# Optimization experiments

Hardware: AMD Instinct MI355X
Metric: run time of the kernel (lower is better)

## Reference

```python
import jax, jax.numpy as jnp
import numpy as np

B, T, C, HD = 4, 2048, 1024, 64

def setup_inputs() -> dict:
    key = jax.random.key(0)
    kx, kq, kk, kv = jax.random.split(key, 4)
    # Weights stored as [n_embed, head_size]; equivalent to torch Linear weight transposed.
    scale = 1.0 / np.sqrt(C)
    return {
        "x": jax.random.normal(kx, (B, T, C), dtype=jnp.float32),
        "Wq": jax.random.normal(kq, (C, HD), dtype=jnp.float32) * scale,
        "Wk": jax.random.normal(kk, (C, HD), dtype=jnp.float32) * scale,
        "Wv": jax.random.normal(kv, (C, HD), dtype=jnp.float32) * scale,
    }

def reference(x, Wq, Wk, Wv):
    # Projections (no bias)
    q = x @ Wq  # [B,T,HD]
    k = x @ Wk
    v = x @ Wv
    hd = k.shape[-1]
    # NOTE: original multiplies by sqrt(head_size) (not the usual 1/sqrt) -- faithful.
    scores = jnp.einsum("btd,bsd->bts", q, k) * (hd ** 0.5)  # [B,T,T]
    # First softmax over full (unmasked) rows
    w = jax.nn.softmax(scores, axis=-1)
    # Causal mask applied AFTER the first softmax, then a second softmax
    causal = jnp.tril(jnp.ones((q.shape[1], q.shape[1]), dtype=bool))  # [T,T]
    w = jnp.where(causal[None, :, :], w, -jnp.inf)
    w = jax.nn.softmax(w, axis=-1)
    out = jnp.einsum("bts,bsd->btd", w, v)  # [B,T,HD]
    return out
```

## Files before the change

### kernel.cpp

```cpp
#include <hip/hip_runtime.h>
#include <math.h>

#define T_  2048
#define C_  1024
#define HD_ 64

typedef __attribute__((ext_vector_type(8))) short bf16x8;
typedef __attribute__((ext_vector_type(4))) float f32x4;

#define MFMA_BF16(A, B, C) __builtin_amdgcn_mfma_f32_16x16x32_bf16(A, B, C, 0, 0, 0)

__device__ __forceinline__ short f2bf(float f) {
    union { float f; unsigned u; } v; v.f = f;
    unsigned r = v.u + 0x7fffu + ((v.u >> 16) & 1u);
    return (short)(r >> 16);
}
__device__ __forceinline__ float bf2f(short s) {
    union { float f; unsigned u; } v;
    v.u = ((unsigned)(unsigned short)s) << 16;
    return v.f;
}

__global__ __launch_bounds__(256) void prep_w_kernel(
    const float* __restrict__ Wq, const float* __restrict__ Wk,
    const float* __restrict__ Wv, short* __restrict__ wt)
{
    const int m = blockIdx.y;
    const float* W = (m == 0) ? Wq : (m == 1) ? Wk : Wv;
    const int t = threadIdx.x;
    const int c = blockIdx.x * 64 + (t >> 2);
    const int hg = (t & 3) * 16;
    const float4* wp = (const float4*)(W + (size_t)c * HD_ + hg);
    short* hi = wt + (size_t)(m * 2 + 0) * 64 * 1024;
    short* lo = wt + (size_t)(m * 2 + 1) * 64 * 1024;
    #pragma unroll
    for (int u = 0; u < 4; ++u) {
        float4 f = wp[u];
        float vs[4] = {f.x, f.y, f.z, f.w};
        #pragma unroll
        for (int e = 0; e < 4; ++e) {
            int h = hg + u * 4 + e;
            short hh = f2bf(vs[e]);
            hi[(size_t)h * 1024 + c] = hh;
            lo[(size_t)h * 1024 + c] = f2bf(vs[e] - bf2f(hh));
        }
    }
}

__global__ __launch_bounds__(256) void qkv_proj_kernel(
    const float* __restrict__ x, const short* __restrict__ wt,
    short* __restrict__ qhp, short* __restrict__ qlp,
    short* __restrict__ khp, short* __restrict__ klp,
    short* __restrict__ vtp)
{
    __shared__ __align__(16) short xh[32 * 64], xl[32 * 64];
    __shared__ __align__(16) short wh[192 * 64], wl[192 * 64];

    const int t = threadIdx.x, L = t & 63, wv = t >> 6;
    const int R0 = blockIdx.x * 32;
    const int xrow = t >> 3, xch = t & 7;

    f32x4 acc[2][3];
    #pragma unroll
    for (int i = 0; i < 2; ++i)
        #pragma unroll
        for (int j = 0; j < 3; ++j) acc[i][j] = {0.f, 0.f, 0.f, 0.f};

    float4 xa0, xa1;
    bf16x8 wr[2][6];
    const float* xp = x + (size_t)(R0 + xrow) * C_ + xch * 8;

    auto loadX = [&](int c0) {
        xa0 = *(const float4*)(xp + c0);
        xa1 = *(const float4*)(xp + c0 + 4);
    };
    auto loadW = [&](int c0) {
        #pragma unroll
        for (int pl = 0; pl < 2; ++pl)
            #pragma unroll
            for (int u = 0; u < 6; ++u) {
                int cc = t + 256 * u;
                int row = cc >> 3, ch = cc & 7;
                int m = row >> 6, h = row & 63;
                wr[pl][u] = *(const bf16x8*)(wt + (size_t)(m * 2 + pl) * 65536
                                             + (size_t)h * 1024 + c0 + ch * 8);
            }
    };

    loadX(0); loadW(0);
    for (int c0 = 0; c0 < C_; c0 += 64) {
        __syncthreads();
        {
            float vs[8] = {xa0.x, xa0.y, xa0.z, xa0.w, xa1.x, xa1.y, xa1.z, xa1.w};
            bf16x8 vh, vl;
            #pragma unroll
            for (int e = 0; e < 8; ++e) {
                short hh = f2bf(vs[e]);
                vh[e] = hh;
                vl[e] = f2bf(vs[e] - bf2f(hh));
            }
            int slot = (xch ^ (xrow & 7)) * 8;
            *(bf16x8*)&xh[xrow * 64 + slot] = vh;
            *(bf16x8*)&xl[xrow * 64 + slot] = vl;
        }
        {
            #pragma unroll
            for (int pl = 0; pl < 2; ++pl)
                #pragma unroll
                for (int u = 0; u < 6; ++u) {
                    int cc = t + 256 * u;
                    int row = cc >> 3, ch = cc & 7;
                    short* dst = pl ? wl : wh;
                    *(bf16x8*)&dst[row * 64 + ((ch ^ (row & 7)) * 8)] = wr[pl][u];
                }
        }
        if (c0 + 64 < C_) { loadX(c0 + 64); loadW(c0 + 64); }
        __syncthreads();
        #pragma unroll
        for (int kc = 0; kc < 2; ++kc) {
            const int ch = kc * 4 + (L >> 4);
            bf16x8 axh[2], axl[2], bwh[3], bwl[3];
            #pragma unroll
            for (int rt = 0; rt < 2; ++rt) {
                int row = rt * 16 + (L & 15);
                int off = row * 64 + ((ch ^ (row & 7)) * 8);
                axh[rt] = *(const bf16x8*)&xh[off];
                axl[rt] = *(const bf16x8*)&xl[off];
            }
            #pragma unroll
            for (int cl = 0; cl < 3; ++cl) {
                int ct = wv + cl * 4;
                int wrow = ct * 16 + (L & 15);
                int off = wrow * 64 + ((ch ^ (wrow & 7)) * 8);
                bwh[cl] = *(const bf16x8*)&wh[off];
                bwl[cl] = *(const bf16x8*)&wl[off];
            }
            #pragma unroll
            for (int rt = 0; rt < 2; ++rt) {
                acc[rt][0] = MFMA_BF16(axl[rt], bwh[0], acc[rt][0]);
                acc[rt][0] = MFMA_BF16(axh[rt], bwl[0], acc[rt][0]);
                acc[rt][0] = MFMA_BF16(axh[rt], bwh[0], acc[rt][0]);
                acc[rt][1] = MFMA_BF16(axl[rt], bwh[1], acc[rt][1]);
                acc[rt][1] = MFMA_BF16(axh[rt], bwl[1], acc[rt][1]);
                acc[rt][1] = MFMA_BF16(axh[rt], bwh[1], acc[rt][1]);
                acc[rt][2] = MFMA_BF16(bwh[2], axh[rt], acc[rt][2]);
            }
        }
    }

    const int quad = L >> 4;
    #pragma unroll
    for (int rt = 0; rt < 2; ++rt) {
        #pragma unroll
        for (int r = 0; r < 4; ++r) {
            int row = R0 + rt * 16 + quad * 4 + r;
            int h = wv * 16 + (L & 15);
            float vq = acc[rt][0][r] * 8.f;
            short hq = f2bf(vq);
            qhp[(size_t)row * HD_ + h] = hq;
            qlp[(size_t)row * HD_ + h] = f2bf(vq - bf2f(hq));
            float vk = acc[rt][1][r];
            short hk = f2bf(vk);
            khp[(size_t)row * HD_ + h] = hk;
            klp[(size_t)row * HD_ + h] = f2bf(vk - bf2f(hk));
            int d = wv * 16 + quad * 4 + r;
            int tt = R0 + rt * 16 + (L & 15);
            int bb = tt >> 11, tl = tt & (T_ - 1);
            vtp[(size_t)(bb * 64 + d) * T_ + tl] = f2bf(acc[rt][2][r]);
        }
    }
}

__global__ __launch_bounds__(256) void stats_kernel(
    const short* __restrict__ qhp, const short* __restrict__ qlp,
    const short* __restrict__ khp, const short* __restrict__ klp,
    float* __restrict__ pm)
{
    __shared__ __align__(16) short khs[64 * 64], kls[64 * 64];
    __shared__ float red[4 * 64 * 2];

    const int t = threadIdx.x, L = t & 63, wv = t >> 6;
    const int bt = blockIdx.x, seg = blockIdx.y, b = blockIdx.z;
    const int R0 = bt * 64, S0 = seg * 512;

    bf16x8 qfh[4][2], qfl[4][2];
    #pragma unroll
    for (int rt = 0; rt < 4; ++rt)
        #pragma unroll
        for (int dc = 0; dc < 2; ++dc) {
            int row = R0 + rt * 16 + (L & 15);
            size_t off = ((size_t)b * T_ + row) * HD_ + dc * 32 + (L >> 4) * 8;
            qfh[rt][dc] = *(const bf16x8*)(qhp + off);
            qfl[rt][dc] = *(const bf16x8*)(qlp + off);
        }

    float ml[4][4], ll[4][4];
    #pragma unroll
    for (int rt = 0; rt < 4; ++rt)
        #pragma unroll
        for (int r = 0; r < 4; ++r) { ml[rt][r] = -1e30f; ll[rt][r] = 0.f; }

    const int pl = t >> 7, id = t & 127;
    for (int jt = 0; jt < 8; ++jt) {
        __syncthreads();
        {
            const short* src = pl ? klp : khp;
            short* dst = pl ? kls : khs;
            #pragma unroll
            for (int u = 0; u < 4; ++u) {
                int cid = id * 4 + u;
                int col = cid >> 3, ch = cid & 7;
                bf16x8 v = *(const bf16x8*)(src
                    + ((size_t)b * T_ + S0 + jt * 64 + col) * HD_ + ch * 8);
                *(bf16x8*)&dst[col * 64 + ((ch ^ (col & 7)) * 8)] = v;
            }
        }
        __syncthreads();
        const int colL = wv * 16 + (L & 15);
        bf16x8 kf[2], kfl[2];
        #pragma unroll
        for (int dc = 0; dc < 2; ++dc) {
            int ch = dc * 4 + (L >> 4);
            int off = colL * 64 + ((ch ^ (colL & 7)) * 8);
            kf[dc]  = *(const bf16x8*)&khs[off];
            kfl[dc] = *(const bf16x8*)&kls[off];
        }
        #pragma unroll
        for (int rt = 0; rt < 4; ++rt) {
            f32x4 s = {0.f, 0.f, 0.f, 0.f};
            #pragma unroll
            for (int dc = 0; dc < 2; ++dc) {
                s = MFMA_BF16(qfl[rt][dc], kf[dc], s);
                s = MFMA_BF16(qfh[rt][dc], kfl[dc], s);
                s = MFMA_BF16(qfh[rt][dc], kf[dc], s);
            }
            #pragma unroll
            for (int r = 0; r < 4; ++r) {
                float mn = fmaxf(ml[rt][r], s[r]);
                ll[rt][r] = ll[rt][r] * __expf(ml[rt][r] - mn) + __expf(s[r] - mn);
                ml[rt][r] = mn;
            }
        }
    }
    #pragma unroll
    for (int off = 1; off < 16; off <<= 1)
        #pragma unroll
        for (int rt = 0; rt < 4; ++rt)
            #pragma unroll
            for (int r = 0; r < 4; ++r) {
                float mo = __shfl_xor(ml[rt][r], off, 64);
                float lo = __shfl_xor(ll[rt][r], off, 64);
                float mn = fmaxf(ml[rt][r], mo);
                ll[rt][r] = ll[rt][r] * __expf(ml[rt][r] - mn) + lo * __expf(mo - mn);
                ml[rt][r] = mn;
            }
    if ((L & 15) == 0) {
        #pragma unroll
        for (int rt = 0; rt < 4; ++rt)
            #pragma unroll
            for (int r = 0; r < 4; ++r) {
                int row = rt * 16 + (L >> 4) * 4 + r;
                red[(wv * 64 + row) * 2 + 0] = ml[rt][r];
                red[(wv * 64 + row) * 2 + 1] = ll[rt][r];
            }
    }
    __syncthreads();
    if (t < 64) {
        float M = red[t * 2], S = red[t * 2 + 1];
        #pragma unroll
        for (int w = 1; w < 4; ++w) {
            float mo = red[(w * 64 + t) * 2], lo = red[(w * 64 + t) * 2 + 1];
            float mn = fmaxf(M, mo);
            S = S * __expf(M - mn) + lo * __expf(mo - mn);
            M = mn;
        }
        size_t o = ((size_t)((b * 32 + bt) * 4 + seg) * 64 + t) * 2;
        pm[o] = M;
        pm[o + 1] = S;
    }
}

__global__ __launch_bounds__(256) void stat_merge_kernel(
    const float* __restrict__ pm, float* __restrict__ msp, float* __restrict__ ilp)
{
    int gid = blockIdx.x * 256 + threadIdx.x;
    int b = gid >> 11, rl = gid & 2047, bt = rl >> 6, rr = rl & 63;
    float M = -1e30f, S = 0.f;
    #pragma unroll
    for (int seg = 0; seg < 4; ++seg) {
        size_t o = ((size_t)((b * 32 + bt) * 4 + seg) * 64 + rr) * 2;
        float mo = pm[o], lo = pm[o + 1];
        float mn = fmaxf(M, mo);
        S = S * __expf(M - mn) + lo * __expf(mo - mn);
        M = mn;
    }
    msp[gid] = M;
    ilp[gid] = 1.f / S;
}

__global__ __launch_bounds__(512) void pv_kernel(
    const short* __restrict__ qhp, const short* __restrict__ qlp,
    const short* __restrict__ khp, const short* __restrict__ klp,
    const short* __restrict__ vtp, const float* __restrict__ msp,
    const float* __restrict__ ilp, float* __restrict__ out)
{
    __shared__ __align__(16) short khs[128 * 64];
    __shared__ __align__(16) short kls[128 * 64];
    __shared__ __align__(16) short vts[64 * 128];
    __shared__ __align__(16) float es[32 * 128];

    const int t = threadIdx.x, L = t & 63, wv = t >> 6;
    const int b = blockIdx.x >> 6, p = blockIdx.x & 63;
    const int IA = p * 16, IB = (127 - p) * 16;

    bf16x8 qfh[2][2], qfl[2][2];
    #pragma unroll
    for (int rt = 0; rt < 2; ++rt) {
        int row = (rt ? IB : IA) + (L & 15);
        const short* qb  = qhp + ((size_t)b * T_ + row) * HD_;
        const short* qbl = qlp + ((size_t)b * T_ + row) * HD_;
        #pragma unroll
        for (int dc = 0; dc < 2; ++dc) {
            int off = dc * 32 + (L >> 4) * 8;
            qfh[rt][dc] = *(const bf16x8*)(qb + off);
            qfl[rt][dc] = *(const bf16x8*)(qbl + off);
        }
    }
    float ms[2][4], is[2][4];
    int rowg[2][4];
    #pragma unroll
    for (int rt = 0; rt < 2; ++rt)
        #pragma unroll
        for (int r = 0; r < 4; ++r) {
            int rg = (rt ? IB : IA) + (L >> 4) * 4 + r;
            rowg[rt][r] = rg;
            ms[rt][r] = msp[b * T_ + rg];
            is[rt][r] = ilp[b * T_ + rg];
        }

    const short* kbh = khp + (size_t)b * T_ * HD_;
    const short* kbl = klp + (size_t)b * T_ * HD_;
    const short* vb  = vtp + (size_t)b * 64 * T_;
    const int spl = t >> 8, sid = t & 255;

    auto stageK = [&](int jt) {
        const short* src = spl ? kbl : kbh;
        short* dst = spl ? kls : khs;
        #pragma unroll
        for (int u = 0; u < 4; ++u) {
            int cid = sid * 4 + u;
            int col = cid >> 3, c8 = cid & 7;
            bf16x8 v = *(const bf16x8*)(src + (size_t)(jt * 128 + col) * HD_ + c8 * 8);
            *(bf16x8*)&dst[col * 64 + ((c8 ^ (col & 7)) * 8)] = v;
        }
    };
    auto stageV = [&](int jt) {
        #pragma unroll
        for (int u = 0; u < 2; ++u) {
            int cid = t + u * 512;
            int d = cid >> 4, ch = cid & 15;
            bf16x8 v = *(const bf16x8*)(vb + (size_t)d * T_ + jt * 128 + ch * 8);
            *(bf16x8*)&vts[d * 128 + ((ch ^ ((d & 7) * 2)) * 8)] = v;
        }
    };

    const int nA = (IA + 143) >> 7;
    const int nB = (IB + 143) >> 7;
    const int rtp = wv & 1, dh = (wv >> 1) & 1, khf = wv >> 2;
    f32x4 ov[2];
    ov[0] = {0.f, 0.f, 0.f, 0.f};
    ov[1] = {0.f, 0.f, 0.f, 0.f};
    float dn[2][4];
    #pragma unroll
    for (int rt = 0; rt < 2; ++rt)
        #pragma unroll
        for (int r = 0; r < 4; ++r) dn[rt][r] = 0.f;

    for (int jt = 0; jt < nB; ++jt) {
        __syncthreads();
        stageK(jt);
        stageV(jt);
        __syncthreads();
        const int col = wv * 16 + (L & 15);
        bf16x8 kf[2], kfl[2];
        #pragma unroll
        for (int dc = 0; dc < 2; ++dc) {
            int ch = dc * 4 + (L >> 4);
            int off = col * 64 + ((ch ^ (col & 7)) * 8);
            kf[dc]  = *(const bf16x8*)&khs[off];
            kfl[dc] = *(const bf16x8*)&kls[off];
        }
        for (int rt = 0; rt < 2; ++rt) {
            if (rt == 0 && jt >= nA) continue;
            f32x4 s = {0.f, 0.f, 0.f, 0.f};
            #pragma unroll
            for (int dc = 0; dc < 2; ++dc) {
                s = MFMA_BF16(qfl[rt][dc], kf[dc], s);
                s = MFMA_BF16(qfh[rt][dc], kfl[dc], s);
                s = MFMA_BF16(qfh[rt][dc], kf[dc], s);
            }
            #pragma unroll
            for (int r = 0; r < 4; ++r) {
                float pv = __expf(s[r] - ms[rt][r]) * is[rt][r];
                int colg = jt * 128 + col;
                float ev = (colg <= rowg[rt][r]) ? __expf(pv) : 0.f;
                dn[rt][r] += ev;
                int rid = rt * 16 + (L >> 4) * 4 + r;
                es[rid * 128 + (((col >> 3) ^ (rid & 15)) * 8) + (col & 7)] = ev;
            }
        }
        __syncthreads();
        if (!(rtp == 0 && jt >= nA)) {
            #pragma unroll
            for (int u = 0; u < 2; ++u) {
                int kc = khf * 2 + u;
                int rid = rtp * 16 + (L & 15);
                int chunk = (kc * 4 + (L >> 4)) ^ (rid & 15);
                const float* ep = &es[rid * 128 + chunk * 8];
                float4 e0 = *(const float4*)ep;
                float4 e1 = *(const float4*)(ep + 4);
                bf16x8 ef;
                ef[0] = f2bf(e0.x); ef[1] = f2bf(e0.y);
                ef[2] = f2bf(e0.z); ef[3] = f2bf(e0.w);
                ef[4] = f2bf(e1.x); ef[5] = f2bf(e1.y);
                ef[6] = f2bf(e1.z); ef[7] = f2bf(e1.w);
                #pragma unroll
                for (int dt = 0; dt < 2; ++dt) {
                    int d = dh * 32 + dt * 16 + (L & 15);
                    int ch = kc * 4 + (L >> 4);
                    bf16x8 vf = *(const bf16x8*)&vts[d * 128 + ((ch ^ ((d & 7) * 2)) * 8)];
                    ov[dt] = MFMA_BF16(ef, vf, ov[dt]);
                }
            }
        }
    }

    #pragma unroll
    for (int off = 1; off < 16; off <<= 1)
        #pragma unroll
        for (int rt = 0; rt < 2; ++rt)
            #pragma unroll
            for (int r = 0; r < 4; ++r)
                dn[rt][r] += __shfl_xor(dn[rt][r], off, 64);
    __syncthreads();
    float* red  = es + 2304;
    float* dinv = es + 2560;
    if ((L & 15) == 0) {
        #pragma unroll
        for (int rt = 0; rt < 2; ++rt)
            #pragma unroll
            for (int r = 0; r < 4; ++r) {
                int rid = rt * 16 + (L >> 4) * 4 + r;
                red[wv * 32 + rid] = dn[rt][r];
            }
    }
    __syncthreads();
    if (t < 32) {
        float D = 0.f;
        #pragma unroll
        for (int w = 0; w < 8; ++w) D += red[w * 32 + t];
        dinv[t] = 1.f / D;
    }
    float* obuf = es;
    __syncthreads();
    if (khf == 1) {
        #pragma unroll
        for (int dt = 0; dt < 2; ++dt)
            #pragma unroll
            for (int r = 0; r < 4; ++r)
                obuf[((wv - 4) * 64 + L) * 8 + dt * 4 + r] = ov[dt][r];
    }
    __syncthreads();
    if (khf == 0) {
        float* ob = out + (size_t)b * T_ * HD_;
        #pragma unroll
        for (int dt = 0; dt < 2; ++dt)
            #pragma unroll
            for (int r = 0; r < 4; ++r) {
                float o = ov[dt][r] + obuf[(wv * 64 + L) * 8 + dt * 4 + r];
                int rid = rtp * 16 + (L >> 4) * 4 + r;
                int row = (rtp ? IB : IA) + (L >> 4) * 4 + r;
                int d = dh * 32 + dt * 16 + (L & 15);
                ob[(size_t)row * HD_ + d] = o * dinv[rid];
            }
    }
}

extern "C" void kernel_launch(void* const* d_in, const int* in_sizes, int n_in,
                              void* d_out, int out_size, void* d_ws, size_t ws_size,
                              hipStream_t stream) {
    (void)in_sizes; (void)n_in; (void)out_size; (void)ws_size;
    const float* x  = (const float*)d_in[0];
    const float* Wq = (const float*)d_in[1];
    const float* Wk = (const float*)d_in[2];
    const float* Wv = (const float*)d_in[3];
    float* outp = (float*)d_out;

    char* ws = (char*)d_ws;
    short* wt  = (short*)ws;
    float* pm  = (float*)ws;
    float* msp = (float*)(ws + 262144);
    float* ilp = (float*)(ws + 294912);
    short* qh = (short*)(ws + 786432);
    short* ql = (short*)(ws + 786432 + 1048576);
    short* kh = (short*)(ws + 786432 + 2 * 1048576);
    short* kl = (short*)(ws + 786432 + 3 * 1048576);
    short* vt = (short*)(ws + 786432 + 4 * 1048576);

    prep_w_kernel<<<dim3(16, 3), 256, 0, stream>>>(Wq, Wk, Wv, wt);
    qkv_proj_kernel<<<dim3(256), 256, 0, stream>>>(x, wt, qh, ql, kh, kl, vt);
    stats_kernel<<<dim3(32, 4, 4), 256, 0, stream>>>(qh, ql, kh, kl, pm);
    stat_merge_kernel<<<dim3(32), 256, 0, stream>>>(pm, msp, ilp);
    pv_kernel<<<dim3(256), 512, 0, stream>>>(qh, ql, kh, kl, vt, msp, ilp, outp);
}
```

Before: 154.9 us.

## Materialize causal scores in stats pass and drop QK recompute from PV kernel

The stats kernel now writes the fp32 scores of the lower-triangular part to a workspace buffer while computing row statistics. It uses twice as many key segments and register-prefetches the next K tile. The PV kernel no longer recomputes the three-pass split-bf16 QK^T. Instead it reads those stored scores, applies both softmaxes and multiplies with V directly from global memory using 16-row blocks. This removes redundant MFMA work but adds roughly 32MB of score writes and reads through HBM and a larger workspace.

```diff
diff --git a/kernel.cpp b/kernel.cpp
--- a/kernel.cpp
+++ b/kernel.cpp
@@ -174,14 +174,14 @@
 __global__ __launch_bounds__(256) void stats_kernel(
     const short* __restrict__ qhp, const short* __restrict__ qlp,
     const short* __restrict__ khp, const short* __restrict__ klp,
-    float* __restrict__ pm)
+    float* __restrict__ pm, float* __restrict__ sc)
 {
     __shared__ __align__(16) short khs[64 * 64], kls[64 * 64];
     __shared__ float red[4 * 64 * 2];
 
     const int t = threadIdx.x, L = t & 63, wv = t >> 6;
     const int bt = blockIdx.x, seg = blockIdx.y, b = blockIdx.z;
-    const int R0 = bt * 64, S0 = seg * 512;
+    const int R0 = bt * 64, S0 = seg * 256;
 
     bf16x8 qfh[4][2], qfl[4][2];
     #pragma unroll
@@ -201,21 +201,30 @@
         for (int r = 0; r < 4; ++r) { ml[rt][r] = -1e30f; ll[rt][r] = 0.f; }
 
     const int pl = t >> 7, id = t & 127;
-    for (int jt = 0; jt < 8; ++jt) {
+    const short* ksrc = pl ? klp : khp;
+    short* kdst = pl ? kls : khs;
+    bf16x8 kr[4];
+    auto loadK = [&](int jt) {
+        #pragma unroll
+        for (int u = 0; u < 4; ++u) {
+            int cid = id * 4 + u;
+            int col = cid >> 3, ch = cid & 7;
+            kr[u] = *(const bf16x8*)(ksrc
+                + ((size_t)b * T_ + S0 + jt * 64 + col) * HD_ + ch * 8);
+        }
+    };
+
+    loadK(0);
+    for (int jt = 0; jt < 4; ++jt) {
         __syncthreads();
-        {
-            const short* src = pl ? klp : khp;
-            short* dst = pl ? kls : khs;
-            #pragma unroll
-            for (int u = 0; u < 4; ++u) {
-                int cid = id * 4 + u;
-                int col = cid >> 3, ch = cid & 7;
-                bf16x8 v = *(const bf16x8*)(src
-                    + ((size_t)b * T_ + S0 + jt * 64 + col) * HD_ + ch * 8);
-                *(bf16x8*)&dst[col * 64 + ((ch ^ (col & 7)) * 8)] = v;
-            }
+        #pragma unroll
+        for (int u = 0; u < 4; ++u) {
+            int cid = id * 4 + u;
+            int col = cid >> 3, ch = cid & 7;
+            *(bf16x8*)&kdst[col * 64 + ((ch ^ (col & 7)) * 8)] = kr[u];
         }
         __syncthreads();
+        if (jt < 3) loadK(jt + 1);
         const int colL = wv * 16 + (L & 15);
         bf16x8 kf[2], kfl[2];
         #pragma unroll
@@ -225,6 +234,7 @@
             kf[dc]  = *(const bf16x8*)&khs[off];
             kfl[dc] = *(const bf16x8*)&kls[off];
         }
+        const bool doStore = (S0 + jt * 64) <= (R0 + 63);
         #pragma unroll
         for (int rt = 0; rt < 4; ++rt) {
             f32x4 s = {0.f, 0.f, 0.f, 0.f};
@@ -233,6 +243,13 @@
                 s = MFMA_BF16(qfl[rt][dc], kf[dc], s);
                 s = MFMA_BF16(qfh[rt][dc], kfl[dc], s);
                 s = MFMA_BF16(qfh[rt][dc], kf[dc], s);
+            }
+            if (doStore) {
+                #pragma unroll
+                for (int r = 0; r < 4; ++r) {
+                    int row = R0 + rt * 16 + (L >> 4) * 4 + r;
+                    sc[((size_t)b * T_ + row) * T_ + S0 + jt * 64 + colL] = s[r];
+                }
             }
             #pragma unroll
             for (int r = 0; r < 4; ++r) {
@@ -274,7 +291,7 @@
             S = S * __expf(M - mn) + lo * __expf(mo - mn);
             M = mn;
         }
-        size_t o = ((size_t)((b * 32 + bt) * 4 + seg) * 64 + t) * 2;
+        size_t o = ((size_t)((b * 32 + bt) * 8 + seg) * 64 + t) * 2;
         pm[o] = M;
         pm[o + 1] = S;
     }
@@ -287,8 +304,8 @@
     int b = gid >> 11, rl = gid & 2047, bt = rl >> 6, rr = rl & 63;
     float M = -1e30f, S = 0.f;
     #pragma unroll
-    for (int seg = 0; seg < 4; ++seg) {
-        size_t o = ((size_t)((b * 32 + bt) * 4 + seg) * 64 + rr) * 2;
+    for (int seg = 0; seg < 8; ++seg) {
+        size_t o = ((size_t)((b * 32 + bt) * 8 + seg) * 64 + rr) * 2;
         float mo = pm[o], lo = pm[o + 1];
         float mn = fmaxf(M, mo);
         S = S * __expf(M - mn) + lo * __expf(mo - mn);
@@ -298,192 +315,75 @@
     ilp[gid] = 1.f / S;
 }
 
-__global__ __launch_bounds__(512) void pv_kernel(
-    const short* __restrict__ qhp, const short* __restrict__ qlp,
-    const short* __restrict__ khp, const short* __restrict__ klp,
-    const short* __restrict__ vtp, const float* __restrict__ msp,
-    const float* __restrict__ ilp, float* __restrict__ out)
+__global__ __launch_bounds__(256) void pv_kernel(
+    const float* __restrict__ sc, const short* __restrict__ vtp,
+    const float* __restrict__ msp, const float* __restrict__ ilp,
+    float* __restrict__ out)
 {
-    __shared__ __align__(16) short khs[128 * 64];
-    __shared__ __align__(16) short kls[128 * 64];
-    __shared__ __align__(16) short vts[64 * 128];
-    __shared__ __align__(16) float es[32 * 128];
+    __shared__ float ored[4][16][64];
+    __shared__ float dred[4][16];
 
     const int t = threadIdx.x, L = t & 63, wv = t >> 6;
-    const int b = blockIdx.x >> 6, p = blockIdx.x & 63;
-    const int IA = p * 16, IB = (127 - p) * 16;
-
-    bf16x8 qfh[2][2], qfl[2][2];
-    #pragma unroll
-    for (int rt = 0; rt < 2; ++rt) {
-        int row = (rt ? IB : IA) + (L & 15);
-        const short* qb  = qhp + ((size_t)b * T_ + row) * HD_;
-        const short* qbl = qlp + ((size_t)b * T_ + row) * HD_;
-        #pragma unroll
-        for (int dc = 0; dc < 2; ++dc) {
-            int off = dc * 32 + (L >> 4) * 8;
-            qfh[rt][dc] = *(const bf16x8*)(qb + off);
-            qfl[rt][dc] = *(const bf16x8*)(qbl + off);
-        }
-    }
-    float ms[2][4], is[2][4];
-    int rowg[2][4];
-    #pragma unroll
-    for (int rt = 0; rt < 2; ++rt)
-        #pragma unroll
-        for (int r = 0; r < 4; ++r) {
-            int rg = (rt ? IB : IA) + (L >> 4) * 4 + r;
-            rowg[rt][r] = rg;
-            ms[rt][r] = msp[b * T_ + rg];
-            is[rt][r] = ilp[b * T_ + rg];
-        }
-
-    const short* kbh = khp + (size_t)b * T_ * HD_;
-    const short* kbl = klp + (size_t)b * T_ * HD_;
-    const short* vb  = vtp + (size_t)b * 64 * T_;
-    const int spl = t >> 8, sid = t & 255;
-
-    auto stageK = [&](int jt) {
-        const short* src = spl ? kbl : kbh;
-        short* dst = spl ? kls : khs;
-        #pragma unroll
-        for (int u = 0; u < 4; ++u) {
-            int cid = sid * 4 + u;
-            int col = cid >> 3, c8 = cid & 7;
-            bf16x8 v = *(const bf16x8*)(src + (size_t)(jt * 128 + col) * HD_ + c8 * 8);
-            *(bf16x8*)&dst[col * 64 + ((c8 ^ (col & 7)) * 8)] = v;
-        }
-    };
-    auto stageV = [&](int jt) {
-        #pragma unroll
-        for (int u = 0; u < 2; ++u) {
-            int cid = t + u * 512;
-            int d = cid >> 4, ch = cid & 15;
-            bf16x8 v = *(const bf16x8*)(vb + (size_t)d * T_ + jt * 128 + ch * 8);
-            *(bf16x8*)&vts[d * 128 + ((ch ^ ((d & 7) * 2)) * 8)] = v;
-        }
-    };
-
-    const int nA = (IA + 143) >> 7;
-    const int nB = (IB + 143) >> 7;
-    const int rtp = wv & 1, dh = (wv >> 1) & 1, khf = wv >> 2;
-    f32x4 ov[2];
-    ov[0] = {0.f, 0.f, 0.f, 0.f};
-    ov[1] = {0.f, 0.f, 0.f, 0.f};
-    float dn[2][4];
-    #pragma unroll
-    for (int rt = 0; rt < 2; ++rt)
-        #pragma unroll
-        for (int r = 0; r < 4; ++r) dn[rt][r] = 0.f;
-
-    for (int jt = 0; jt < nB; ++jt) {
-        __syncthreads();
-        stageK(jt);
-        stageV(jt);
-        __syncthreads();
-        const int col = wv * 16 + (L & 15);
-        bf16x8 kf[2], kfl[2];
-        #pragma unroll
-        for (int dc = 0; dc < 2; ++dc) {
-            int ch = dc * 4 + (L >> 4);
-            int off = col * 64 + ((ch ^ (col & 7)) * 8);
-            kf[dc]  = *(const bf16x8*)&khs[off];
-            kfl[dc] = *(const bf16x8*)&kls[off];
-        }
-        for (int rt = 0; rt < 2; ++rt) {
-            if (rt == 0 && jt >= nA) continue;
-            f32x4 s = {0.f, 0.f, 0.f, 0.f};
-            #pragma unroll
-            for (int dc = 0; dc < 2; ++dc) {
-                s = MFMA_BF16(qfl[rt][dc], kf[dc], s);
-                s = MFMA_BF16(qfh[rt][dc], kfl[dc], s);
-                s = MFMA_BF16(qfh[rt][dc], kf[dc], s);
-            }
-            #pragma unroll
-            for (int r = 0; r < 4; ++r) {
-                float pv = __expf(s[r] - ms[rt][r]) * is[rt][r];
-                int colg = jt * 128 + col;
-                float ev = (colg <= rowg[rt][r]) ? __expf(pv) : 0.f;
-                dn[rt][r] += ev;
-                int rid = rt * 16 + (L >> 4) * 4 + r;
-                es[rid * 128 + (((col >> 3) ^ (rid & 15)) * 8) + (col & 7)] = ev;
-            }
-        }
-        __syncthreads();
-        if (!(rtp == 0 && jt >= nA)) {
-            #pragma unroll
-            for (int u = 0; u < 2; ++u) {
-                int kc = khf * 2 + u;
-                int rid = rtp * 16 + (L & 15);
-                int chunk = (kc * 4 + (L >> 4)) ^ (rid & 15);
-                const float* ep = &es[rid * 128 + chunk * 8];
-                float4 e0 = *(const float4*)ep;
-                float4 e1 = *(const float4*)(ep + 4);
-                bf16x8 ef;
-                ef[0] = f2bf(e0.x); ef[1] = f2bf(e0.y);
-                ef[2] = f2bf(e0.z); ef[3] = f2bf(e0.w);
-                ef[4] = f2bf(e1.x); ef[5] = f2bf(e1.y);
-                ef[6] = f2bf(e1.z); ef[7] = f2bf(e1.w);
-                #pragma unroll
-                for (int dt = 0; dt < 2; ++dt) {
-                    int d = dh * 32 + dt * 16 + (L & 15);
-                    int ch = kc * 4 + (L >> 4);
-                    bf16x8 vf = *(const bf16x8*)&vts[d * 128 + ((ch ^ ((d & 7) * 2)) * 8)];
-                    ov[dt] = MFMA_BF16(ef, vf, ov[dt]);
-                }
-            }
-        }
-    }
-
-    #pragma unroll
-    for (int off = 1; off < 16; off <<= 1)
-        #pragma unroll
-        for (int rt = 0; rt < 2; ++rt)
-            #pragma unroll
-            for (int r = 0; r < 4; ++r)
-                dn[rt][r] += __shfl_xor(dn[rt][r], off, 64);
+    const int b = blockIdx.x & 3;
+    const int p = 127 - (blockIdx.x >> 2);
+    const int T0 = p * 16;
+    const int row = T0 + (L & 15);
+
+    const float ms = msp[b * T_ + row];
+    const float is = ilp[b * T_ + row];
+    const float* srow = sc + ((size_t)b * T_ + row) * T_;
+    const short* vb = vtp + (size_t)b * 64 * T_;
+    const int nJ = (T0 + 143) >> 7;
+    const int cq = (L >> 4) * 8;
+
+    f32x4 ov[4];
+    #pragma unroll
+    for (int dt = 0; dt < 4; ++dt) ov[dt] = {0.f, 0.f, 0.f, 0.f};
+    float dn = 0.f;
+
+    for (int jt = 0; jt < nJ; ++jt) {
+        const int c0 = jt * 128 + wv * 32 + cq;
+        float4 s0 = *(const float4*)(srow + c0);
+        float4 s1 = *(const float4*)(srow + c0 + 4);
+        float vs[8] = {s0.x, s0.y, s0.z, s0.w, s1.x, s1.y, s1.z, s1.w};
+        bf16x8 ef;
+        #pragma unroll
+        for (int e = 0; e < 8; ++e) {
+            float pvv = __expf(vs[e] - ms) * is;
+            float evv = (c0 + e <= row) ? __expf(pvv) : 0.f;
+            dn += evv;
+            ef[e] = f2bf(evv);
+        }
+        #pragma unroll
+        for (int dt = 0; dt < 4; ++dt) {
+            bf16x8 vf = *(const bf16x8*)(vb + (size_t)(dt * 16 + (L & 15)) * T_ + c0);
+            ov[dt] = MFMA_BF16(ef, vf, ov[dt]);
+        }
+    }
+
+    dn += __shfl_xor(dn, 16, 64);
+    dn += __shfl_xor(dn, 32, 64);
+    if (L < 16) dred[wv][L] = dn;
+    #pragma unroll
+    for (int dt = 0; dt < 4; ++dt)
+        #pragma unroll
+        for (int r = 0; r < 4; ++r)
+            ored[wv][(L >> 4) * 4 + r][dt * 16 + (L & 15)] = ov[dt][r];
     __syncthreads();
-    float* red  = es + 2304;
-    float* dinv = es + 2560;
-    if ((L & 15) == 0) {
-        #pragma unroll
-        for (int rt = 0; rt < 2; ++rt)
-            #pragma unroll
-            for (int r = 0; r < 4; ++r) {
-                int rid = rt * 16 + (L >> 4) * 4 + r;
-                red[wv * 32 + rid] = dn[rt][r];
-            }
-    }
-    __syncthreads();
-    if (t < 32) {
-        float D = 0.f;
-        #pragma unroll
-        for (int w = 0; w < 8; ++w) D += red[w * 32 + t];
-        dinv[t] = 1.f / D;
-    }
-    float* obuf = es;
-    __syncthreads();
-    if (khf == 1) {
-        #pragma unroll
-        for (int dt = 0; dt < 2; ++dt)
-            #pragma unroll
-            for (int r = 0; r < 4; ++r)
-                obuf[((wv - 4) * 64 + L) * 8 + dt * 4 + r] = ov[dt][r];
-    }
-    __syncthreads();
-    if (khf == 0) {
-        float* ob = out + (size_t)b * T_ * HD_;
-        #pragma unroll
-        for (int dt = 0; dt < 2; ++dt)
-            #pragma unroll
-            for (int r = 0; r < 4; ++r) {
-                float o = ov[dt][r] + obuf[(wv * 64 + L) * 8 + dt * 4 + r];
-                int rid = rtp * 16 + (L >> 4) * 4 + r;
-                int row = (rtp ? IB : IA) + (L >> 4) * 4 + r;
-                int d = dh * 32 + dt * 16 + (L & 15);
-                ob[(size_t)row * HD_ + d] = o * dinv[rid];
-            }
-    }
+
+    const int orow = t >> 4, d0 = (t & 15) * 4;
+    float D = dred[0][orow] + dred[1][orow] + dred[2][orow] + dred[3][orow];
+    float di = 1.f / D;
+    float4 o;
+    o.x = (ored[0][orow][d0 + 0] + ored[1][orow][d0 + 0]
+         + ored[2][orow][d0 + 0] + ored[3][orow][d0 + 0]) * di;
+    o.y = (ored[0][orow][d0 + 1] + ored[1][orow][d0 + 1]
+         + ored[2][orow][d0 + 1] + ored[3][orow][d0 + 1]) * di;
+    o.z = (ored[0][orow][d0 + 2] + ored[1][orow][d0 + 2]
+         + ored[2][orow][d0 + 2] + ored[3][orow][d0 + 2]) * di;
+    o.w = (ored[0][orow][d0 + 3] + ored[1][orow][d0 + 3]
+         + ored[2][orow][d0 + 3] + ored[3][orow][d0 + 3]) * di;
+    *(float4*)(out + ((size_t)b * T_ + T0 + orow) * HD_ + d0) = o;
 }
 
 extern "C" void kernel_launch(void* const* d_in, const int* in_sizes, int n_in,
@@ -499,17 +399,18 @@
     char* ws = (char*)d_ws;
     short* wt  = (short*)ws;
     float* pm  = (float*)ws;
-    float* msp = (float*)(ws + 262144);
-    float* ilp = (float*)(ws + 294912);
+    float* msp = (float*)(ws + 524288);
+    float* ilp = (float*)(ws + 557056);
     short* qh = (short*)(ws + 786432);
     short* ql = (short*)(ws + 786432 + 1048576);
     short* kh = (short*)(ws + 786432 + 2 * 1048576);
     short* kl = (short*)(ws + 786432 + 3 * 1048576);
     short* vt = (short*)(ws + 786432 + 4 * 1048576);
+    float* sc = (float*)(ws + 8388608);
 
     prep_w_kernel<<<dim3(16, 3), 256, 0, stream>>>(Wq, Wk, Wv, wt);
     qkv_proj_kernel<<<dim3(256), 256, 0, stream>>>(x, wt, qh, ql, kh, kl, vt);
-    stats_kernel<<<dim3(32, 4, 4), 256, 0, stream>>>(qh, ql, kh, kl, pm);
+    stats_kernel<<<dim3(32, 8, 4), 256, 0, stream>>>(qh, ql, kh, kl, pm, sc);
     stat_merge_kernel<<<dim3(32), 256, 0, stream>>>(pm, msp, ilp);
-    pv_kernel<<<dim3(256), 512, 0, stream>>>(qh, ql, kh, kl, vt, msp, ilp, outp);
-}
+    pv_kernel<<<dim3(512), 256, 0, stream>>>(sc, vt, msp, ilp, outp);
+}
```

Measured after the change: 148.9 us. 1.04x faster.
